# Optimization experiments

Hardware: AMD Instinct MI355X
Metric: run time of the kernel (lower is better)

Reference implementation:

```python
import jax, jax.numpy as jnp
import numpy as np

HEADS = 16
HEAD_DIM = 64

def setup_inputs() -> dict:
    key = jax.random.key(0)
    ks = jax.random.split(key, 5)
    S, B, H = 1024, 4, 1024
    scale = 1.0 / np.sqrt(H)
    return {
        "hidden_states": jax.random.normal(ks[0], (S, B, H), jnp.float32),
        "attention_mask": jnp.zeros((B * HEADS, 1, S), jnp.float32),
        "Wq": jax.random.normal(ks[1], (H, H), jnp.float32) * scale,
        "bq": jnp.zeros((H,), jnp.float32),
        "Wk": jax.random.normal(ks[2], (H, H), jnp.float32) * scale,
        "bk": jnp.zeros((H,), jnp.float32),
        "Wv": jax.random.normal(ks[3], (H, H), jnp.float32) * scale,
        "bv": jnp.zeros((H,), jnp.float32),
    }

def reference(hidden_states, attention_mask, Wq, bq, Wk, bk, Wv, bv):
    S, B, H = hidden_states.shape
    d = HEAD_DIM
    inv_sqrt_d = 1.0 / np.sqrt(d)
    # QKV projections (torch Linear: x @ W.T + b)
    q = hidden_states @ Wq.T + bq  # (S, B, H)
    k = hidden_states @ Wk.T + bk
    v = hidden_states @ Wv.T + bv
    # (S, B*heads, d) -> (B*heads, S, d)
    q = q.reshape(S, B * HEADS, d).transpose(1, 0, 2)
    k = k.reshape(S, B * HEADS, d).transpose(1, 0, 2)
    v = v.reshape(S, B * HEADS, d).transpose(1, 0, 2)
    # SDDMM: scaled scores + additive mask -> (B*heads, S, S)
    scores = jnp.einsum('nsd,ntd->nst', q, k) * inv_sqrt_d + attention_mask
    probs = jax.nn.softmax(scores, axis=-1)
    # AV bmm -> (B*heads, S, d); note: dropout in source is seeded but never applied
    ctx = jnp.einsum('nst,ntd->nsd', probs, v)
    # back to (S, B, hidden)
    ctx = ctx.transpose(1, 0, 2).reshape(S, B, H)
    return ctx
```

## Files before the change

### kernel.cpp

```cpp
#include <hip/hip_runtime.h>
#include <hip/hip_bf16.h>
#include <math.h>

#define S_LEN 1024
#define BATCH 4
#define HID 1024
#define NHEADS 16
#define DHEAD 64
#define NTOT 64
#define M_ROWS 4096

typedef unsigned short u16;
typedef unsigned int u32;
typedef __bf16 bf16x8 __attribute__((ext_vector_type(8)));
typedef float f32x4 __attribute__((ext_vector_type(4)));

__device__ __forceinline__ u16 f2bf(float x) {
    __hip_bfloat16 h = __float2bfloat16(x);
    return *(u16*)&h;
}

__device__ __forceinline__ float fexp2(float x) {
#if __has_builtin(__builtin_amdgcn_exp2f)
    return __builtin_amdgcn_exp2f(x);
#else
    return __expf(x * 0.6931471805599453f);
#endif
}

__device__ __forceinline__ void gll16(const u16* g, u16* l) {
    __builtin_amdgcn_global_load_lds(
        (const __attribute__((address_space(1))) u32*)g,
        (__attribute__((address_space(3))) u32*)l, 16, 0, 0);
}

__global__ __launch_bounds__(256) void cvt_all(
    const float* __restrict__ X, const float* __restrict__ wq,
    const float* __restrict__ wk, const float* __restrict__ wv,
    u16* __restrict__ Xb, u16* __restrict__ Wb)
{
    const int bid = blockIdx.x;
    const float* src;
    u16* dst;
    size_t off;
    if (bid < 4096) {
        src = X; dst = Xb; off = (size_t)bid * 1024;
    } else {
        const int wb = bid - 4096;
        const int which = wb >> 10;
        src = (which == 0) ? wq : (which == 1) ? wk : wv;
        dst = Wb + (size_t)which * HID * HID;
        off = (size_t)(wb & 1023) * 1024;
    }
    const size_t idx = off + threadIdx.x * 4;
    float4 x = *(const float4*)(src + idx);
    *(ushort4*)(dst + idx) = make_ushort4(f2bf(x.x), f2bf(x.y), f2bf(x.z), f2bf(x.w));
}

__global__ __launch_bounds__(256, 3) void qkv_mfma(
    const u16* __restrict__ Xb, const u16* __restrict__ Wb,
    const float* __restrict__ bq, const float* __restrict__ bk,
    const float* __restrict__ bv,
    u16* __restrict__ Qb, u16* __restrict__ Kb, u16* __restrict__ VT)
{
    const int m0 = blockIdx.x * 128;
    const int n0 = blockIdx.y * 128;
    const int which = blockIdx.z;

    __shared__ __align__(16) u16 As[128 * 64];
    __shared__ __align__(16) u16 Bs[128 * 64];

    const int tid = threadIdx.x;
    const int lane = tid & 63;
    const int w = tid >> 6;
    const int wm = w & 1, wn = w >> 1;
    const int quad = lane >> 4;
    const int l15 = lane & 15;
    const int r7 = l15 & 7;

    const u16* W = Wb + (size_t)which * HID * HID;

    f32x4 acc[4][4];
    #pragma unroll
    for (int i = 0; i < 4; ++i)
        #pragma unroll
        for (int j = 0; j < 4; ++j)
            #pragma unroll
            for (int r = 0; r < 4; ++r) acc[i][j][r] = 0.0f;

    const int srow = lane >> 3;
    const int scg  = ((lane & 7) ^ srow) * 8;

    for (int k0 = 0; k0 < HID; k0 += 64) {
        #pragma unroll
        for (int c = 0; c < 4; ++c) {
            const int seg = w * 4 + c;
            const int row = seg * 8 + srow;
            gll16(Xb + (size_t)(m0 + row) * HID + k0 + scg, As + seg * 512);
            gll16(W  + (size_t)(n0 + row) * HID + k0 + scg, Bs + seg * 512);
        }
        __syncthreads();

        #pragma unroll
        for (int kk = 0; kk < 2; ++kk) {
            const int xo = ((kk * 4 + quad) ^ r7) * 8;
            bf16x8 af[4], bf[4];
            #pragma unroll
            for (int i = 0; i < 4; ++i)
                af[i] = *(const bf16x8*)(As + (wm * 64 + i * 16 + l15) * 64 + xo);
            #pragma unroll
            for (int j = 0; j < 4; ++j)
                bf[j] = *(const bf16x8*)(Bs + (wn * 64 + j * 16 + l15) * 64 + xo);
            #pragma unroll
            for (int i = 0; i < 4; ++i)
                #pragma unroll
                for (int j = 0; j < 4; ++j)
                    acc[i][j] = __builtin_amdgcn_mfma_f32_16x16x32_bf16(
                        af[i], bf[j], acc[i][j], 0, 0, 0);
        }
        __syncthreads();
    }

    const float* bias = (which == 0) ? bq : (which == 1) ? bk : bv;
    #pragma unroll
    for (int j = 0; j < 4; ++j) {
        const int o = n0 + wn * 64 + j * 16 + l15;
        const float bias_v = bias[o];
        const int head = o >> 6, d = o & 63;
        #pragma unroll
        for (int i = 0; i < 4; ++i) {
            const int mbase = m0 + wm * 64 + i * 16 + quad * 4;
            const int s = mbase >> 2;
            #pragma unroll
            for (int r = 0; r < 4; ++r) {
                const int n = r * NHEADS + head;
                const u16 hv = f2bf(acc[i][j][r] + bias_v);
                if (which == 0)
                    Qb[((size_t)n * S_LEN + s) * DHEAD + d] = hv;
                else if (which == 1)
                    Kb[((size_t)n * S_LEN + s) * DHEAD + d] = hv;
                else
                    VT[(size_t)n * (DHEAD * S_LEN) + (size_t)d * S_LEN + s] = hv;
            }
        }
    }
}

__global__ __launch_bounds__(256, 3) void attn_mfma(
    const u16* __restrict__ Qb, const u16* __restrict__ Kb,
    const u16* __restrict__ VT, const float* __restrict__ mask,
    float* __restrict__ out)
{
    const int bid = blockIdx.x;
    const int swz = (bid & 7) * 128 + (bid >> 3);
    const int n = swz >> 4;
    const int s0 = (swz & 15) * 64;
    const int b = n >> 4, head = n & 15;

    __shared__ __align__(16) char smem[46080];
    u16* Kbuf = (u16*)smem;
    u16* Vbuf = (u16*)(smem + 16384);
    u16* Ps   = (u16*)(smem + 32768);
    float* Ms = (float*)(smem + 41984);
    float* Of = (float*)smem;

    const int tid = threadIdx.x;
    const int lane = tid & 63;
    const int w = tid >> 6;
    const int quad = lane >> 4;
    const int l15 = lane & 15;
    const size_t nbase = (size_t)n * S_LEN * DHEAD;

    const float LOG2E = 1.44269504f;
    const float SCL2  = 0.18033688f;
    const float MOFF  = -23.0831099f;

    const int xs0 = ((quad ^ (l15 & 7)) * 8);
    const int xs1 = (((4 + quad) ^ (l15 & 7)) * 8);

    const int srow = lane >> 3;
    const int scg  = (lane & 7) ^ (srow & 7);

    {
        float4 mv = *(const float4*)(mask + (size_t)n * S_LEN + tid * 4);
        Ms[tid * 4 + 0] = fmaf(mv.x, LOG2E, MOFF);
        Ms[tid * 4 + 1] = fmaf(mv.y, LOG2E, MOFF);
        Ms[tid * 4 + 2] = fmaf(mv.z, LOG2E, MOFF);
        Ms[tid * 4 + 3] = fmaf(mv.w, LOG2E, MOFF);
    }

    const int q = w * 16 + l15;
    bf16x8 qf[2];
    #pragma unroll
    for (int st = 0; st < 2; ++st)
        qf[st] = *(const bf16x8*)(Qb + nbase +
            (size_t)(s0 + q) * 64 + st * 32 + quad * 8);

    f32x4 O[4];
    float l_lane = 0.0f;
    #pragma unroll
    for (int jt = 0; jt < 4; ++jt)
        #pragma unroll
        for (int r = 0; r < 4; ++r) O[jt][r] = 0.0f;

    {
        #pragma unroll
        for (int c = 0; c < 2; ++c) {
            const int seg = w * 2 + c;
            const int row = seg * 8 + srow;
            gll16(Kb + nbase + (size_t)row * 64 + scg * 8, Kbuf + seg * 512);
            gll16(VT + nbase + (size_t)row * S_LEN + scg * 8, Vbuf + seg * 512);
        }
    }
    __syncthreads();

    for (int it = 0; it < 16; ++it) {
        const int t0 = it * 64;
        const u16* kb = Kbuf + (it & 1) * 4096;
        const u16* vb = Vbuf + (it & 1) * 4096;

        if (it < 15) {
            u16* kd = Kbuf + ((it + 1) & 1) * 4096;
            u16* vd = Vbuf + ((it + 1) & 1) * 4096;
            #pragma unroll
            for (int c = 0; c < 2; ++c) {
                const int seg = w * 2 + c;
                const int row = seg * 8 + srow;
                gll16(Kb + nbase + (size_t)(t0 + 64 + row) * 64 + scg * 8, kd + seg * 512);
                gll16(VT + nbase + (size_t)row * S_LEN + t0 + 64 + scg * 8, vd + seg * 512);
            }
        }

        f32x4 sc[4];
        #pragma unroll
        for (int j = 0; j < 4; ++j)
            #pragma unroll
            for (int r = 0; r < 4; ++r) sc[j][r] = 0.0f;

        __builtin_amdgcn_s_setprio(1);
        #pragma unroll
        for (int st = 0; st < 2; ++st) {
            const int xo = st ? xs1 : xs0;
            bf16x8 kf[4];
            #pragma unroll
            for (int j = 0; j < 4; ++j)
                kf[j] = *(const bf16x8*)(kb + (j * 16 + l15) * 64 + xo);
            #pragma unroll
            for (int j = 0; j < 4; ++j)
                sc[j] = __builtin_amdgcn_mfma_f32_16x16x32_bf16(
                    kf[j], qf[st], sc[j], 0, 0, 0);
        }
        __builtin_amdgcn_s_setprio(0);

        #pragma unroll
        for (int j = 0; j < 4; ++j) {
            float4 mb = *(const float4*)(Ms + t0 + j * 16 + quad * 4);
            const float p0 = fexp2(fmaf(sc[j][0], SCL2, mb.x));
            const float p1 = fexp2(fmaf(sc[j][1], SCL2, mb.y));
            const float p2 = fexp2(fmaf(sc[j][2], SCL2, mb.z));
            const float p3 = fexp2(fmaf(sc[j][3], SCL2, mb.w));
            l_lane += (p0 + p1) + (p2 + p3);
            *(ushort4*)(Ps + q * 72 + j * 16 + quad * 4) =
                make_ushort4(f2bf(p0), f2bf(p1), f2bf(p2), f2bf(p3));
        }

        __builtin_amdgcn_s_setprio(1);
        #pragma unroll
        for (int st = 0; st < 2; ++st) {
            const int xo = st ? xs1 : xs0;
            bf16x8 vf[4];
            #pragma unroll
            for (int jt = 0; jt < 4; ++jt)
                vf[jt] = *(const bf16x8*)(vb + (jt * 16 + l15) * 64 + xo);
            bf16x8 pf = *(const bf16x8*)(Ps + q * 72 + st * 32 + quad * 8);
            #pragma unroll
            for (int jt = 0; jt < 4; ++jt)
                O[jt] = __builtin_amdgcn_mfma_f32_16x16x32_bf16(
                    vf[jt], pf, O[jt], 0, 0, 0);
        }
        __builtin_amdgcn_s_setprio(0);

        __syncthreads();
    }

    float l = l_lane;
    l += __shfl_xor(l, 16);
    l += __shfl_xor(l, 32);
    const float inv_l = 1.0f / l;
    __syncthreads();

    #pragma unroll
    for (int jt = 0; jt < 4; ++jt)
        #pragma unroll
        for (int r = 0; r < 4; ++r)
            Of[q * 72 + jt * 16 + quad * 4 + r] = O[jt][r] * inv_l;
    __syncthreads();

    const int tx = tid & 15, ty = tid >> 4;
    #pragma unroll
    for (int p = 0; p < 4; ++p) {
        const int qq = p * 16 + ty;
        float4 v = *(const float4*)(Of + qq * 72 + tx * 4);
        *(float4*)(out + (size_t)(s0 + qq) * (BATCH * HID) + (size_t)b * HID +
                   head * DHEAD + tx * 4) = v;
    }
}

extern "C" void kernel_launch(void* const* d_in, const int* in_sizes, int n_in,
                              void* d_out, int out_size, void* d_ws, size_t ws_size,
                              hipStream_t stream)
{
    const float* X    = (const float*)d_in[0];
    const float* mask = (const float*)d_in[1];
    const float* Wq   = (const float*)d_in[2];
    const float* bq   = (const float*)d_in[3];
    const float* Wk   = (const float*)d_in[4];
    const float* bk   = (const float*)d_in[5];
    const float* Wv   = (const float*)d_in[6];
    const float* bv   = (const float*)d_in[7];
    float* out = (float*)d_out;

    const size_t MX = (size_t)M_ROWS * HID;
    const size_t MW = (size_t)HID * HID;
    u16* wsp = (u16*)d_ws;
    u16* Xb = wsp;
    u16* Wb = Xb + MX;
    u16* Qb = Wb + 3 * MW;
    u16* Kb = Qb + MX;
    u16* VT = Kb + MX;

    cvt_all<<<dim3(4096 + 3072), 256, 0, stream>>>(X, Wq, Wk, Wv, Xb, Wb);
    qkv_mfma<<<dim3(M_ROWS / 128, HID / 128, 3), 256, 0, stream>>>(
        Xb, Wb, bq, bk, bv, Qb, Kb, VT);
    attn_mfma<<<dim3(S_LEN / 64 * NTOT), 256, 0, stream>>>(Qb, Kb, VT, mask, out);
}
```

Before: 156.8 us.

## Keep softmax probabilities in registers via permlane16 swap instead of LDS round-trip

Packs the exp'd probabilities into bf16 pairs with v_cvt_pk_bf16_f32 and rearranges them across lanes with v_permlane16_swap so they feed the PV MFMA directly as the B operand. This removes the Ps shared-memory buffer and its store/load round-trip. The V-fragment LDS offsets are permuted to match the new k ordering. The smaller LDS footprint lets occupancy rise to 4 blocks per SM via launch_bounds, which adds register pressure risk.

```diff
diff --git a/kernel.cpp b/kernel.cpp
--- a/kernel.cpp
+++ b/kernel.cpp
@@ -26,6 +26,16 @@
 #else
     return __expf(x * 0.6931471805599453f);
 #endif
+}
+
+__device__ __forceinline__ u32 cvtpk(float a, float b) {
+    u32 r;
+    asm("v_cvt_pk_bf16_f32 %0, %1, %2" : "=v"(r) : "v"(a), "v"(b));
+    return r;
+}
+
+__device__ __forceinline__ void pl16swap(u32& a, u32& b) {
+    asm("v_permlane16_swap_b32 %0, %1" : "+v"(a), "+v"(b));
 }
 
 __device__ __forceinline__ void gll16(const u16* g, u16* l) {
@@ -146,7 +156,7 @@
     }
 }
 
-__global__ __launch_bounds__(256, 3) void attn_mfma(
+__global__ __launch_bounds__(256, 4) void attn_mfma(
     const u16* __restrict__ Qb, const u16* __restrict__ Kb,
     const u16* __restrict__ VT, const float* __restrict__ mask,
     float* __restrict__ out)
@@ -157,11 +167,10 @@
     const int s0 = (swz & 15) * 64;
     const int b = n >> 4, head = n & 15;
 
-    __shared__ __align__(16) char smem[46080];
+    __shared__ __align__(16) char smem[36864];
     u16* Kbuf = (u16*)smem;
     u16* Vbuf = (u16*)(smem + 16384);
-    u16* Ps   = (u16*)(smem + 32768);
-    float* Ms = (float*)(smem + 41984);
+    float* Ms = (float*)(smem + 32768);
     float* Of = (float*)smem;
 
     const int tid = threadIdx.x;
@@ -169,14 +178,18 @@
     const int w = tid >> 6;
     const int quad = lane >> 4;
     const int l15 = lane & 15;
+    const int r7 = l15 & 7;
     const size_t nbase = (size_t)n * S_LEN * DHEAD;
 
     const float LOG2E = 1.44269504f;
     const float SCL2  = 0.18033688f;
     const float MOFF  = -23.0831099f;
 
-    const int xs0 = ((quad ^ (l15 & 7)) * 8);
-    const int xs1 = (((4 + quad) ^ (l15 & 7)) * 8);
+    const int xs0 = ((quad ^ r7) * 8);
+    const int xs1 = (((4 + quad) ^ r7) * 8);
+    const int qperm = ((quad & 1) << 1) | (quad >> 1);
+    const int xv0 = ((qperm ^ r7) * 8);
+    const int xv1 = (((4 + qperm) ^ r7) * 8);
 
     const int srow = lane >> 3;
     const int scg  = (lane & 7) ^ (srow & 7);
@@ -252,31 +265,41 @@
         }
         __builtin_amdgcn_s_setprio(0);
 
+        float pj[4][4];
         #pragma unroll
         for (int j = 0; j < 4; ++j) {
             float4 mb = *(const float4*)(Ms + t0 + j * 16 + quad * 4);
-            const float p0 = fexp2(fmaf(sc[j][0], SCL2, mb.x));
-            const float p1 = fexp2(fmaf(sc[j][1], SCL2, mb.y));
-            const float p2 = fexp2(fmaf(sc[j][2], SCL2, mb.z));
-            const float p3 = fexp2(fmaf(sc[j][3], SCL2, mb.w));
-            l_lane += (p0 + p1) + (p2 + p3);
-            *(ushort4*)(Ps + q * 72 + j * 16 + quad * 4) =
-                make_ushort4(f2bf(p0), f2bf(p1), f2bf(p2), f2bf(p3));
-        }
+            pj[j][0] = fexp2(fmaf(sc[j][0], SCL2, mb.x));
+            pj[j][1] = fexp2(fmaf(sc[j][1], SCL2, mb.y));
+            pj[j][2] = fexp2(fmaf(sc[j][2], SCL2, mb.z));
+            pj[j][3] = fexp2(fmaf(sc[j][3], SCL2, mb.w));
+            l_lane += (pj[j][0] + pj[j][1]) + (pj[j][2] + pj[j][3]);
+        }
+        u32 W00 = cvtpk(pj[0][0], pj[0][1]), W01 = cvtpk(pj[0][2], pj[0][3]);
+        u32 W10 = cvtpk(pj[1][0], pj[1][1]), W11 = cvtpk(pj[1][2], pj[1][3]);
+        u32 W20 = cvtpk(pj[2][0], pj[2][1]), W21 = cvtpk(pj[2][2], pj[2][3]);
+        u32 W30 = cvtpk(pj[3][0], pj[3][1]), W31 = cvtpk(pj[3][2], pj[3][3]);
+        pl16swap(W00, W10); pl16swap(W01, W11);
+        pl16swap(W20, W30); pl16swap(W21, W31);
+        u32 pw[2][4];
+        pw[0][0] = W00; pw[0][1] = W01; pw[0][2] = W10; pw[0][3] = W11;
+        pw[1][0] = W20; pw[1][1] = W21; pw[1][2] = W30; pw[1][3] = W31;
 
         __builtin_amdgcn_s_setprio(1);
         #pragma unroll
         for (int st = 0; st < 2; ++st) {
-            const int xo = st ? xs1 : xs0;
+            const int xo = st ? xv1 : xv0;
             bf16x8 vf[4];
             #pragma unroll
             for (int jt = 0; jt < 4; ++jt)
                 vf[jt] = *(const bf16x8*)(vb + (jt * 16 + l15) * 64 + xo);
-            bf16x8 pf = *(const bf16x8*)(Ps + q * 72 + st * 32 + quad * 8);
+            union { u32 wds[4]; bf16x8 v; } pu;
+            pu.wds[0] = pw[st][0]; pu.wds[1] = pw[st][1];
+            pu.wds[2] = pw[st][2]; pu.wds[3] = pw[st][3];
             #pragma unroll
             for (int jt = 0; jt < 4; ++jt)
                 O[jt] = __builtin_amdgcn_mfma_f32_16x16x32_bf16(
-                    vf[jt], pf, O[jt], 0, 0, 0);
+                    vf[jt], pu.v, O[jt], 0, 0, 0);
         }
         __builtin_amdgcn_s_setprio(0);
 
```

Result: faster. 148.6 us (-5.2%).
